# Kernel optimization log

Measured on AMD Instinct MI355X. Metric: run time of the kernel, lower is better.

The kernel has to match this reference:

```python
import jax, jax.numpy as jnp
import numpy as np

B, N, FD = 2, 50000, 13
E = 250000
M, H = 128, 128          # message_dim, hidden_dim
EDGE_IN = 2 * FD + 8     # 34
NODE_IN = FD + 2 * M     # 269


def _mlp(x, w1, b1, w2, b2):
    return jnp.tanh(x @ w1 + b1) @ w2 + b2


def setup_inputs() -> dict:
    root = jax.random.key(0)
    k = lambda i: jax.random.fold_in(root, i)

    def lin(i, din, dout):
        w = jax.random.normal(k(i), (din, dout), jnp.float32) * np.float32(1.0 / np.sqrt(din))
        b = jax.random.normal(k(i + 100), (dout,), jnp.float32) * np.float32(0.01)
        return w, b

    ew1, eb1 = lin(1, EDGE_IN, H); ew2, eb2 = lin(2, H, M)      # mlp_edge
    ww1, wb1 = lin(3, EDGE_IN, H); ww2, wb2 = lin(4, H, 1)      # mlp_weight
    xw1, xb1 = lin(5, EDGE_IN, H); xw2, xb2 = lin(6, H, M)      # mlp_edge_world
    yw1, yb1 = lin(7, EDGE_IN, H); yw2, yb2 = lin(8, H, 1)      # mlp_weight_world
    nw1, nb1 = lin(9, NODE_IN, H); nw2, nb2 = lin(10, H, FD)    # mlp_node

    z_h = jax.random.normal(k(20), (B, N, FD), jnp.float32)
    edge_hh = jax.random.randint(k(21), (B, 2, E), 0, N, jnp.int32)
    edge_world = jax.random.randint(k(22), (B, 2, E), 0, N, jnp.int32)
    return dict(z_h=z_h, edge_hh=edge_hh, edge_world=edge_world,
                ew1=ew1, eb1=eb1, ew2=ew2, eb2=eb2,
                ww1=ww1, wb1=wb1, ww2=ww2, wb2=wb2,
                xw1=xw1, xb1=xb1, xw2=xw2, xb2=xb2,
                yw1=yw1, yb1=yb1, yw2=yw2, yb2=yb2,
                nw1=nw1, nb1=nb1, nw2=nw2, nb2=nb2)


def _edge_features(z, s, t):
    # z: (N, FD); s, t: (E,)
    pos, vel = z[:, 0:3], z[:, 3:6]
    diff = pos[s] - pos[t]                               # (E, 3)
    dist = jnp.sum(diff * diff, axis=-1, keepdims=True)  # (E, 1) squared distance
    vxc = jnp.cross(vel[s], vel[t])                      # (E, 3)
    vxn = jnp.linalg.norm(vxc, axis=-1, keepdims=True)   # (E, 1)
    return jnp.concatenate([diff, dist, vxc, vxn], axis=-1)  # (E, 8)


def reference(z_h, edge_hh, edge_world,
              ew1, eb1, ew2, eb2, ww1, wb1, ww2, wb2,
              xw1, xb1, xw2, xb2, yw1, yb1, yw2, yb2,
              nw1, nb1, nw2, nb2):
    n_nodes = z_h.shape[1]

    def per_batch(z, e_hh, e_w):
        # normal edges
        s, t = e_hh[0], e_hh[1]
        inp = jnp.concatenate([z[s], z[t], _edge_features(z, s, t)], axis=-1)  # (E, 34)
        m = _mlp(inp, ew1, eb1, ew2, eb2)                                       # (E, M)
        w = jax.nn.sigmoid(_mlp(inp, ww1, wb1, ww2, wb2))                       # (E, 1)
        agg_h = jnp.zeros((n_nodes, M), z.dtype).at[t].add(w * m)
        # world edges
        sw, tw = e_w[0], e_w[1]
        inpw = jnp.concatenate([z[sw], z[tw], _edge_features(z, sw, tw)], axis=-1)
        mw = _mlp(inpw, xw1, xb1, xw2, xb2)
        ww_ = jax.nn.sigmoid(_mlp(inpw, yw1, yb1, yw2, yb2))
        agg_w = jnp.zeros((n_nodes, M), z.dtype).at[tw].add(ww_ * mw)
        return agg_h, agg_w

    m_agg_h, m_agg_w = jax.vmap(per_batch)(z_h, edge_hh, edge_world)  # (B, N, M) each
    input_node = jnp.concatenate([z_h, m_agg_h, m_agg_w], axis=-1)    # (B, N, 269)
    delta_z_h = _mlp(input_node, nw1, nb1, nw2, nb2)                  # (B, N, 13)
    return delta_z_h
```

## Files before the change

kernel.cpp:

```cpp
#include <hip/hip_runtime.h>
#include <hip/hip_bf16.h>

#define B_   2
#define N_   50000
#define FD_  13
#define E_   250000
#define M_   128
#define H_   128

typedef __attribute__((ext_vector_type(8))) short  short8;
typedef __attribute__((ext_vector_type(8))) __bf16 bf16x8;
typedef __attribute__((ext_vector_type(4))) float  f32x4;
typedef __attribute__((ext_vector_type(4))) unsigned int uint4v;
typedef __attribute__((ext_vector_type(8))) unsigned short ushort8;

#define AGG_BYTES  (4ull * N_ * 128 * 4)
#define HIST_BYTES (4ull * N_ * 4)
#define SORT_BYTES (4ull * E_ * 4)
#define OFF_EW1 0u
#define OFF_WW1 8192u
#define OFF_EW2 16384u
#define OFF_XW1 32768u
#define OFF_YW1 40960u
#define OFF_XW2 49152u
#define OFF_NW1 65536u
#define OFF_NW2 102400u

__device__ __forceinline__ float bf2f(unsigned short u) {
    unsigned int v = ((unsigned int)u) << 16;
    return __builtin_bit_cast(float, v);
}
__device__ __forceinline__ unsigned short f2bf(float f) {
    __bf16 h = (__bf16)f;
    return __builtin_bit_cast(unsigned short, h);
}
__device__ __forceinline__ float tanh_fast(float x) {
    float e = __builtin_amdgcn_exp2f(x * 2.8853900817779268f);
    float r = __builtin_amdgcn_rcpf(e + 1.0f);
    return __builtin_fmaf(-2.0f, r, 1.0f);
}
__device__ __forceinline__ float sigmoid_fast(float x) {
    float e = __builtin_amdgcn_exp2f(x * -1.4426950408889634f);
    return __builtin_amdgcn_rcpf(1.0f + e);
}
__device__ __forceinline__ f32x4 mfma16(short8 a, short8 b, f32x4 c) {
    return __builtin_amdgcn_mfma_f32_16x16x32_bf16(
        __builtin_bit_cast(bf16x8, a), __builtin_bit_cast(bf16x8, b), c, 0, 0, 0);
}

__global__ void prep_kernel(const float* __restrict__ ew1, const float* __restrict__ ww1,
                            const float* __restrict__ ew2, const float* __restrict__ xw1,
                            const float* __restrict__ yw1, const float* __restrict__ xw2,
                            const float* __restrict__ nw1, const float* __restrict__ nw2,
                            unsigned short* __restrict__ fb, uint4v* __restrict__ hist4) {
    int m = blockIdx.y, f = blockIdx.x, l = threadIdx.x;
    {
        unsigned int flat = ((unsigned int)m * gridDim.x + (unsigned int)f) * 64u + (unsigned int)l;
        const uint4v zv = {0u, 0u, 0u, 0u};
        for (unsigned int i = flat; i < 50000u; i += gridDim.x * gridDim.y * 64u)
            hist4[i] = zv;
    }
    const float* src; int K, Nn, KS; unsigned int off;
    switch (m) {
        case 0: src = ew1; K = 34;  Nn = 128; KS = 2; off = OFF_EW1; break;
        case 1: src = ww1; K = 34;  Nn = 128; KS = 2; off = OFF_WW1; break;
        case 2: src = ew2; K = 128; Nn = 128; KS = 4; off = OFF_EW2; break;
        case 3: src = xw1; K = 34;  Nn = 128; KS = 2; off = OFF_XW1; break;
        case 4: src = yw1; K = 34;  Nn = 128; KS = 2; off = OFF_YW1; break;
        case 5: src = xw2; K = 128; Nn = 128; KS = 4; off = OFF_XW2; break;
        case 6: src = nw1; K = 269; Nn = 128; KS = 9; off = OFF_NW1; break;
        default: src = nw2; K = 128; Nn = 13; KS = 4; off = OFF_NW2; break;
    }
    int NT = (Nn + 15) / 16;
    if (f >= KS * NT) return;
    int ks = f / NT, nt = f % NT;
    int n = nt * 16 + (l & 15);
    unsigned short* dst = fb + off + ((unsigned int)f * 64u + (unsigned int)l) * 8u;
    #pragma unroll
    for (int j = 0; j < 8; j++) {
        int k = ks * 32 + ((l >> 4) * 8) + j;
        int kk = k; bool valid = (k < K) && (n < Nn);
        if (m == 6) {
            if (k < 256)      kk = k + 13;
            else if (k < 269) kk = k - 256;
            else              valid = false;
            valid = valid && (n < Nn);
        }
        dst[j] = valid ? f2bf(src[kk * Nn + n]) : (unsigned short)0;
    }
}

__global__ void hist_kernel(const int* __restrict__ ehh, const int* __restrict__ eww,
                            int* __restrict__ hist) {
    int p = blockIdx.y, idx = blockIdx.x * 256 + threadIdx.x;
    if (idx >= E_) return;
    const int* eg = ((p >> 1) ? eww : ehh) + (size_t)(p & 1) * 2 * E_;
    atomicAdd(&hist[p * N_ + eg[E_ + idx]], 1);
}

__global__ void scan_kernel(int* __restrict__ hist) {
    __shared__ int part[1024];
    const int p = blockIdx.x, tid = threadIdx.x;
    int* h = hist + p * N_;
    const int lo = tid * 52;
    int cnt = N_ - lo; if (cnt < 0) cnt = 0; if (cnt > 52) cnt = 52;
    int v[52];
    int sum = 0;
    if (cnt == 52) {
        const int4* src = (const int4*)(h + lo);
        #pragma unroll
        for (int i = 0; i < 13; i++) {
            int4 t = src[i];
            v[4*i] = t.x; v[4*i+1] = t.y; v[4*i+2] = t.z; v[4*i+3] = t.w;
        }
        #pragma unroll
        for (int i = 0; i < 52; i++) sum += v[i];
    } else {
        for (int i = 0; i < cnt; i++) sum += h[lo + i];
    }
    part[tid] = sum;
    __syncthreads();
    for (int off = 1; off < 1024; off <<= 1) {
        int t = (tid >= off) ? part[tid - off] : 0;
        __syncthreads();
        part[tid] += t;
        __syncthreads();
    }
    int excl = (tid == 0) ? 0 : part[tid - 1];
    if (cnt == 52) {
        int4* dst = (int4*)(h + lo);
        #pragma unroll
        for (int i = 0; i < 13; i++) {
            int4 o;
            o.x = excl; excl += v[4*i];
            o.y = excl; excl += v[4*i+1];
            o.z = excl; excl += v[4*i+2];
            o.w = excl; excl += v[4*i+3];
            dst[i] = o;
        }
    } else {
        for (int i = 0; i < cnt; i++) { int t = h[lo + i]; h[lo + i] = excl; excl += t; }
    }
}

__global__ void scatter_kernel(const int* __restrict__ ehh, const int* __restrict__ eww,
                               int* __restrict__ hist, unsigned int* __restrict__ sorted,
                               uint4v* __restrict__ agg4) {
    int p = blockIdx.y, idx = blockIdx.x * 256 + threadIdx.x;
    {
        unsigned int flat = ((unsigned int)p * gridDim.x + (unsigned int)blockIdx.x) * 256u
                          + (unsigned int)threadIdx.x;
        const unsigned int nthr = gridDim.x * gridDim.y * 256u;
        const uint4v zv = {0u, 0u, 0u, 0u};
        for (unsigned int i = flat; i < 6400000u; i += nthr) agg4[i] = zv;
    }
    if (idx >= E_) return;
    const int* eg = ((p >> 1) ? eww : ehh) + (size_t)(p & 1) * 2 * E_;
    int s = eg[idx];
    int t = eg[E_ + idx];
    int pos = atomicAdd(&hist[p * N_ + t], 1);
    sorted[(size_t)p * E_ + pos] = (unsigned int)s | ((unsigned int)t << 16);
}

__launch_bounds__(256, 3)
__global__ void edge_kernel_agg(const float* __restrict__ z,
                                const unsigned int* __restrict__ sorted,
                                const unsigned short* __restrict__ fb,
                                float* __restrict__ agg,
                                const float* __restrict__ eb1, const float* __restrict__ wb1,
                                const float* __restrict__ ww2, const float* __restrict__ wb2,
                                const float* __restrict__ eb2,
                                const float* __restrict__ xb1, const float* __restrict__ yb1,
                                const float* __restrict__ yw2, const float* __restrict__ yb2,
                                const float* __restrict__ xb2) {
    __shared__ alignas(16) unsigned short Abuf[128][48];
    __shared__ alignas(16) unsigned short Hbuf[128][136];
    __shared__ float w_acc[128];
    __shared__ int   tgt_s[128];

    const int tid  = threadIdx.x;
    const int lane = tid & 63, wv = tid >> 6, quad = lane >> 4, c = lane & 15;
    const int pass = blockIdx.y, b = pass & 1, set = pass >> 1;
    const int ebase = blockIdx.x * 128;

    const float* zb = z + (size_t)b * N_ * FD_;
    float* aggp = agg + (size_t)pass * N_ * 128;

    const short8* Fm1 = (const short8*)(fb + (set ? OFF_XW1 : OFF_EW1));
    const short8* Fw1 = (const short8*)(fb + (set ? OFF_YW1 : OFF_WW1));
    const short8* Fm2 = (const short8*)(fb + (set ? OFF_XW2 : OFF_EW2));
    const float* B1m = set ? xb1 : eb1;
    const float* B1w = set ? yb1 : wb1;
    const float* B2m = set ? xb2 : eb2;
    const float* Wv2 = set ? yw2 : ww2;
    const float wbias = (set ? yb2 : wb2)[0];

    const int nt0 = wv * 2;
    short8 bm[2][2], bw[2][2], b2f[2][4];
    float bias1m[2], bias1w[2], bias2m[2], w2v[2];
    #pragma unroll
    for (int i = 0; i < 2; i++) {
        int nt = nt0 + i, n = nt * 16 + c;
        #pragma unroll
        for (int ks = 0; ks < 2; ks++) { bm[i][ks] = Fm1[(ks * 8 + nt) * 64 + lane];
                                         bw[i][ks] = Fw1[(ks * 8 + nt) * 64 + lane]; }
        #pragma unroll
        for (int ks = 0; ks < 4; ks++) { b2f[i][ks] = Fm2[(ks * 8 + nt) * 64 + lane]; }
        bias1m[i] = B1m[n]; bias1w[i] = B1w[n];
        bias2m[i] = B2m[n]; w2v[i] = Wv2[n];
    }

    if (tid < 128) {
        const int e = tid;
        const int prt = e >> 4, pqd = (e >> 2) & 3, prr = e & 3;
        const int wpos = pqd * 32 + prt * 4 + prr;
        int sp = ebase + wpos;
        const bool valid = (sp < E_);
        if (!valid) sp = E_ - 1;
        unsigned int st = sorted[(size_t)pass * E_ + sp];
        int s = (int)(st & 0xffffu), t = (int)(st >> 16);
        tgt_s[e] = valid ? t : -1;
        w_acc[e] = 0.0f;
        const float* zs = zb + (size_t)s * 13;
        const float* zt = zb + (size_t)t * 13;
        float fs[13], ft[13];
        __builtin_memcpy(fs, zs, 13 * sizeof(float));
        __builtin_memcpy(ft, zt, 13 * sizeof(float));
        float d0 = fs[0] - ft[0], d1 = fs[1] - ft[1], d2 = fs[2] - ft[2];
        float dist = d0 * d0 + d1 * d1 + d2 * d2;
        float c0 = fs[4] * ft[5] - fs[5] * ft[4];
        float c1 = fs[5] * ft[3] - fs[3] * ft[5];
        float c2 = fs[3] * ft[4] - fs[4] * ft[3];
        float vxn = sqrtf(c0 * c0 + c1 * c1 + c2 * c2);
        unsigned short row[40];
        #pragma unroll
        for (int j = 0; j < 13; j++) { row[j] = f2bf(fs[j]); row[13 + j] = f2bf(ft[j]); }
        row[26] = f2bf(d0); row[27] = f2bf(d1); row[28] = f2bf(d2); row[29] = f2bf(dist);
        row[30] = f2bf(c0); row[31] = f2bf(c1); row[32] = f2bf(c2); row[33] = f2bf(vxn);
        #pragma unroll
        for (int j = 34; j < 40; j++) row[j] = 0;
        #pragma unroll
        for (int v = 0; v < 5; v++) {
            short8 sv;
            #pragma unroll
            for (int j = 0; j < 8; j++) sv[j] = (short)row[v * 8 + j];
            *((short8*)&Abuf[e][v * 8]) = sv;
        }
    }
    __syncthreads();

    #pragma unroll 4
    for (int rt = 0; rt < 8; rt++) {
        const unsigned short* ar = &Abuf[rt * 16 + c][0];
        short8 a0 = *((const short8*)(ar + quad * 8));
        short8 a1 = {};
        if (quad == 0) a1 = *((const short8*)(ar + 32));
        float wpart[4] = {0.f, 0.f, 0.f, 0.f};
        #pragma unroll
        for (int i = 0; i < 2; i++) {
            f32x4 accm = {bias1m[i], bias1m[i], bias1m[i], bias1m[i]};
            f32x4 accw = {bias1w[i], bias1w[i], bias1w[i], bias1w[i]};
            accm = mfma16(a0, bm[i][0], accm);
            accm = mfma16(a1, bm[i][1], accm);
            accw = mfma16(a0, bw[i][0], accw);
            accw = mfma16(a1, bw[i][1], accw);
            int n = (nt0 + i) * 16 + c;
            #pragma unroll
            for (int r = 0; r < 4; r++) {
                Hbuf[rt * 16 + quad * 4 + r][n] = f2bf(tanh_fast(accm[r]));
                wpart[r] += tanh_fast(accw[r]) * w2v[i];
            }
        }
        #pragma unroll
        for (int r = 0; r < 4; r++) {
            float v = wpart[r];
            v += __shfl_xor(v, 1); v += __shfl_xor(v, 2);
            v += __shfl_xor(v, 4); v += __shfl_xor(v, 8);
            if (c == r) atomicAdd(&w_acc[rt * 16 + quad * 4 + r], v);
        }
    }
    __syncthreads();
    if (tid < 128) w_acc[tid] = sigmoid_fast(w_acc[tid] + wbias);
    __syncthreads();

    {
        const int n0 = nt0 * 16 + c;
        const int n1 = n0 + 16;
        int   tp = -1;
        float va0 = 0.f, va1 = 0.f;
        bool  from_start = true;
        #pragma unroll 2
        for (int rt = 0; rt < 8; rt++) {
            const unsigned short* hr = &Hbuf[rt * 16 + c][0];
            short8 h0 = *((const short8*)(hr + quad * 8));
            short8 h1 = *((const short8*)(hr + 32 + quad * 8));
            short8 h2 = *((const short8*)(hr + 64 + quad * 8));
            short8 h3 = *((const short8*)(hr + 96 + quad * 8));
            f32x4 accA = {bias2m[0], bias2m[0], bias2m[0], bias2m[0]};
            f32x4 accB = {bias2m[1], bias2m[1], bias2m[1], bias2m[1]};
            accA = mfma16(h0, b2f[0][0], accA);
            accA = mfma16(h1, b2f[0][1], accA);
            accA = mfma16(h2, b2f[0][2], accA);
            accA = mfma16(h3, b2f[0][3], accA);
            accB = mfma16(h0, b2f[1][0], accB);
            accB = mfma16(h1, b2f[1][1], accB);
            accB = mfma16(h2, b2f[1][2], accB);
            accB = mfma16(h3, b2f[1][3], accB);
            const int elq = rt * 16 + quad * 4;
            #pragma unroll
            for (int r = 0; r < 4; r++) {
                const int row = elq + r;
                const int tg = tgt_s[row];
                const float g = w_acc[row];
                const float v0 = accA[r] * g;
                const float v1 = accB[r] * g;
                if (tg == tp) {
                    va0 += v0; va1 += v1;
                } else {
                    if (tp >= 0) {
                        float* dst = aggp + (size_t)tp * 128;
                        if (from_start) { atomicAdd(dst + n0, va0); atomicAdd(dst + n1, va1); }
                        else            { dst[n0] = va0; dst[n1] = va1; }
                    }
                    tp = tg; va0 = v0; va1 = v1;
                    from_start = (rt == 0 && r == 0);
                }
            }
        }
        if (tp >= 0) {
            float* dst = aggp + (size_t)tp * 128;
            atomicAdd(dst + n0, va0);
            atomicAdd(dst + n1, va1);
        }
    }
}

#define NODE_BLOCKS 1024
__launch_bounds__(256, 4)
__global__ void node_fused(const float* __restrict__ z,
                           const float* __restrict__ agg,
                           const unsigned short* __restrict__ fb,
                           const float* __restrict__ nb1,
                           const float* __restrict__ nb2,
                           float* __restrict__ out) {
    __shared__ alignas(16) unsigned short Abuf[2][16][296];
    __shared__ alignas(16) unsigned short Hbuf[16][136];

    const int tid  = threadIdx.x;
    const int lane = tid & 63, wv = tid >> 6, quad = lane >> 4, c = lane & 15;
    const int nl = tid >> 4, part = tid & 15;
    constexpr int NT_TILES = (B_ * N_) / 16;

    for (int j = tid; j < 2 * 16 * 19; j += 256) {
        int bufi = j / (16 * 19), jj = j % (16 * 19);
        Abuf[bufi][jj / 19][269 + jj % 19] = 0;
    }

    const short8* F1 = (const short8*)(fb + OFF_NW1);
    const short8* F2 = (const short8*)(fb + OFF_NW2);
    const int nt0 = wv * 2;
    const float b1a = nb1[nt0 * 16 + c];
    const float b1b = nb1[(nt0 + 1) * 16 + c];
    const float bias2 = (c < 13) ? nb2[c] : 0.0f;

    f32x4 pa0, pa1, pb0, pb1;
    float pz = 0.0f;

    int t = blockIdx.x;

    {
        const int g = t * 16 + nl;
        const int b = (g >= N_) ? 1 : 0;
        const int tt = g - b * N_;
        const float* ap0 = agg + ((size_t)b * N_ + tt) * 128 + part * 8;
        const float* ap1 = agg + ((size_t)(2 + b) * N_ + tt) * 128 + part * 8;
        pa0 = *(const f32x4*)(ap0); pa1 = *(const f32x4*)(ap0 + 4);
        pb0 = *(const f32x4*)(ap1); pb1 = *(const f32x4*)(ap1 + 4);
        if (tid < 208) pz = z[(size_t)(t * 16 + tid / 13) * 13 + (tid % 13)];
    }

    int buf = 0;
    for (; t < NT_TILES; t += NODE_BLOCKS) {
        const int g0 = t * 16;
        {
            ushort8 u;
            #pragma unroll
            for (int k = 0; k < 4; k++) { u[k] = f2bf(pa0[k]); u[4 + k] = f2bf(pa1[k]); }
            *((ushort8*)&Abuf[buf][nl][part * 8]) = u;
            #pragma unroll
            for (int k = 0; k < 4; k++) { u[k] = f2bf(pb0[k]); u[4 + k] = f2bf(pb1[k]); }
            *((ushort8*)&Abuf[buf][nl][128 + part * 8]) = u;
            if (tid < 208) Abuf[buf][tid / 13][256 + tid % 13] = f2bf(pz);
        }
        const int tn = t + NODE_BLOCKS;
        if (tn < NT_TILES) {
            const int g = tn * 16 + nl;
            const int b = (g >= N_) ? 1 : 0;
            const int tt = g - b * N_;
            const float* ap0 = agg + ((size_t)b * N_ + tt) * 128 + part * 8;
            const float* ap1 = agg + ((size_t)(2 + b) * N_ + tt) * 128 + part * 8;
            pa0 = *(const f32x4*)(ap0); pa1 = *(const f32x4*)(ap0 + 4);
            pb0 = *(const f32x4*)(ap1); pb1 = *(const f32x4*)(ap1 + 4);
            if (tid < 208) pz = z[(size_t)(tn * 16 + tid / 13) * 13 + (tid % 13)];
        }
        __syncthreads();

        {
            f32x4 acc0 = {b1a, b1a, b1a, b1a};
            f32x4 acc1 = {b1b, b1b, b1b, b1b};
            #pragma unroll
            for (int ks = 0; ks < 9; ks++) {
                short8 a = *((const short8*)(&Abuf[buf][c][0] + ks * 32 + quad * 8));
                acc0 = mfma16(a, F1[(ks * 8 + nt0) * 64 + lane], acc0);
                acc1 = mfma16(a, F1[(ks * 8 + nt0 + 1) * 64 + lane], acc1);
            }
            #pragma unroll
            for (int r = 0; r < 4; r++) {
                Hbuf[quad * 4 + r][nt0 * 16 + c]       = f2bf(tanh_fast(acc0[r]));
                Hbuf[quad * 4 + r][(nt0 + 1) * 16 + c] = f2bf(tanh_fast(acc1[r]));
            }
        }
        __syncthreads();

        if (wv == 0) {
            f32x4 acc = {bias2, bias2, bias2, bias2};
            #pragma unroll
            for (int ks = 0; ks < 4; ks++) {
                short8 h = *((const short8*)(&Hbuf[c][0] + ks * 32 + quad * 8));
                acc = mfma16(h, F2[ks * 64 + lane], acc);
            }
            #pragma unroll
            for (int r = 0; r < 4; r++) {
                int g = g0 + quad * 4 + r;
                if (c < 13) out[(size_t)g * 13 + c] = acc[r];
            }
        }
        buf ^= 1;
    }
}

extern "C" void kernel_launch(void* const* d_in, const int* in_sizes, int n_in,
                              void* d_out, int out_size, void* d_ws, size_t ws_size,
                              hipStream_t stream) {
    const float* z   = (const float*)d_in[0];
    const int* ehh   = (const int*)d_in[1];
    const int* eww   = (const int*)d_in[2];
    const float* ew1 = (const float*)d_in[3];
    const float* eb1 = (const float*)d_in[4];
    const float* ew2 = (const float*)d_in[5];
    const float* eb2 = (const float*)d_in[6];
    const float* ww1 = (const float*)d_in[7];
    const float* wb1 = (const float*)d_in[8];
    const float* ww2 = (const float*)d_in[9];
    const float* wb2 = (const float*)d_in[10];
    const float* xw1 = (const float*)d_in[11];
    const float* xb1 = (const float*)d_in[12];
    const float* xw2 = (const float*)d_in[13];
    const float* xb2 = (const float*)d_in[14];
    const float* yw1 = (const float*)d_in[15];
    const float* yb1 = (const float*)d_in[16];
    const float* yw2 = (const float*)d_in[17];
    const float* yb2 = (const float*)d_in[18];
    const float* nw1 = (const float*)d_in[19];
    const float* nb1 = (const float*)d_in[20];
    const float* nw2 = (const float*)d_in[21];
    const float* nb2 = (const float*)d_in[22];

    float* agg  = (float*)d_ws;
    int* hist   = (int*)((char*)d_ws + AGG_BYTES);
    unsigned int* sorted = (unsigned int*)((char*)d_ws + AGG_BYTES + HIST_BYTES);
    unsigned short* frag = (unsigned short*)((char*)d_ws + AGG_BYTES + HIST_BYTES + SORT_BYTES);

    prep_kernel<<<dim3(72, 8), 64, 0, stream>>>(ew1, ww1, ew2, xw1, yw1, xw2, nw1, nw2,
                                                frag, (uint4v*)hist);
    hist_kernel<<<dim3((E_ + 255) / 256, 4), 256, 0, stream>>>(ehh, eww, hist);
    scan_kernel<<<4, 1024, 0, stream>>>(hist);
    scatter_kernel<<<dim3((E_ + 255) / 256, 4), 256, 0, stream>>>(ehh, eww, hist, sorted,
                                                                  (uint4v*)agg);
    edge_kernel_agg<<<dim3((E_ + 127) / 128, 4), 256, 0, stream>>>(
        z, sorted, frag, agg,
        eb1, wb1, ww2, wb2, eb2,
        xb1, yb1, yw2, yb2, xb2);
    node_fused<<<NODE_BLOCKS, 256, 0, stream>>>(
        z, agg, frag, nb1, nb2, (float*)d_out);
}
```

Baseline: 396.0 us.

## Split edge gate MLP into separate kernel writing per-edge gates

Moves the sigmoid-gated weight MLP out of the fused edge kernel into a new gate_kernel that writes one gate value per sorted edge to a workspace buffer. The main edge kernel then reads that gate instead of computing it, which cuts its register and instruction load and may raise occupancy. In exchange the edge gather and feature build run twice, there is one extra launch, and the gates take an extra round trip through global memory.

```diff
diff --git a/kernel.cpp b/kernel.cpp
--- a/kernel.cpp
+++ b/kernel.cpp
@@ -17,6 +17,7 @@
 #define AGG_BYTES  (4ull * N_ * 128 * 4)
 #define HIST_BYTES (4ull * N_ * 4)
 #define SORT_BYTES (4ull * E_ * 4)
+#define GATE_BYTES (4ull * E_ * 4)
 #define OFF_EW1 0u
 #define OFF_WW1 8192u
 #define OFF_EW2 16384u
@@ -162,21 +163,17 @@
     sorted[(size_t)p * E_ + pos] = (unsigned int)s | ((unsigned int)t << 16);
 }
 
-__launch_bounds__(256, 3)
-__global__ void edge_kernel_agg(const float* __restrict__ z,
-                                const unsigned int* __restrict__ sorted,
-                                const unsigned short* __restrict__ fb,
-                                float* __restrict__ agg,
-                                const float* __restrict__ eb1, const float* __restrict__ wb1,
-                                const float* __restrict__ ww2, const float* __restrict__ wb2,
-                                const float* __restrict__ eb2,
-                                const float* __restrict__ xb1, const float* __restrict__ yb1,
-                                const float* __restrict__ yw2, const float* __restrict__ yb2,
-                                const float* __restrict__ xb2) {
+__launch_bounds__(256, 6)
+__global__ void gate_kernel(const float* __restrict__ z,
+                            const unsigned int* __restrict__ sorted,
+                            const unsigned short* __restrict__ fb,
+                            float* __restrict__ gate_g,
+                            const float* __restrict__ wb1, const float* __restrict__ ww2,
+                            const float* __restrict__ wb2,
+                            const float* __restrict__ yb1, const float* __restrict__ yw2,
+                            const float* __restrict__ yb2) {
     __shared__ alignas(16) unsigned short Abuf[128][48];
-    __shared__ alignas(16) unsigned short Hbuf[128][136];
     __shared__ float w_acc[128];
-    __shared__ int   tgt_s[128];
 
     const int tid  = threadIdx.x;
     const int lane = tid & 63, wv = tid >> 6, quad = lane >> 4, c = lane & 15;
@@ -184,30 +181,20 @@
     const int ebase = blockIdx.x * 128;
 
     const float* zb = z + (size_t)b * N_ * FD_;
-    float* aggp = agg + (size_t)pass * N_ * 128;
-
-    const short8* Fm1 = (const short8*)(fb + (set ? OFF_XW1 : OFF_EW1));
     const short8* Fw1 = (const short8*)(fb + (set ? OFF_YW1 : OFF_WW1));
-    const short8* Fm2 = (const short8*)(fb + (set ? OFF_XW2 : OFF_EW2));
-    const float* B1m = set ? xb1 : eb1;
     const float* B1w = set ? yb1 : wb1;
-    const float* B2m = set ? xb2 : eb2;
     const float* Wv2 = set ? yw2 : ww2;
     const float wbias = (set ? yb2 : wb2)[0];
 
     const int nt0 = wv * 2;
-    short8 bm[2][2], bw[2][2], b2f[2][4];
-    float bias1m[2], bias1w[2], bias2m[2], w2v[2];
+    short8 bw[2][2];
+    float bias1w[2], w2v[2];
     #pragma unroll
     for (int i = 0; i < 2; i++) {
         int nt = nt0 + i, n = nt * 16 + c;
         #pragma unroll
-        for (int ks = 0; ks < 2; ks++) { bm[i][ks] = Fm1[(ks * 8 + nt) * 64 + lane];
-                                         bw[i][ks] = Fw1[(ks * 8 + nt) * 64 + lane]; }
-        #pragma unroll
-        for (int ks = 0; ks < 4; ks++) { b2f[i][ks] = Fm2[(ks * 8 + nt) * 64 + lane]; }
-        bias1m[i] = B1m[n]; bias1w[i] = B1w[n];
-        bias2m[i] = B2m[n]; w2v[i] = Wv2[n];
+        for (int ks = 0; ks < 2; ks++) bw[i][ks] = Fw1[(ks * 8 + nt) * 64 + lane];
+        bias1w[i] = B1w[n]; w2v[i] = Wv2[n];
     }
 
     if (tid < 128) {
@@ -215,11 +202,9 @@
         const int prt = e >> 4, pqd = (e >> 2) & 3, prr = e & 3;
         const int wpos = pqd * 32 + prt * 4 + prr;
         int sp = ebase + wpos;
-        const bool valid = (sp < E_);
-        if (!valid) sp = E_ - 1;
+        if (sp >= E_) sp = E_ - 1;
         unsigned int st = sorted[(size_t)pass * E_ + sp];
         int s = (int)(st & 0xffffu), t = (int)(st >> 16);
-        tgt_s[e] = valid ? t : -1;
         w_acc[e] = 0.0f;
         const float* zs = zb + (size_t)s * 13;
         const float* zt = zb + (size_t)t * 13;
@@ -249,38 +234,134 @@
     }
     __syncthreads();
 
+    #pragma unroll 1
+    for (int rt = 0; rt < 8; rt++) {
+        const unsigned short* ar = &Abuf[rt * 16 + c][0];
+        short8 a0 = *((const short8*)(ar + quad * 8));
+        short8 a1 = {};
+        if (quad == 0) a1 = *((const short8*)(ar + 32));
+        float wpart[4] = {0.f, 0.f, 0.f, 0.f};
+        #pragma unroll
+        for (int i = 0; i < 2; i++) {
+            f32x4 accw = {bias1w[i], bias1w[i], bias1w[i], bias1w[i]};
+            accw = mfma16(a0, bw[i][0], accw);
+            accw = mfma16(a1, bw[i][1], accw);
+            #pragma unroll
+            for (int r = 0; r < 4; r++) wpart[r] += tanh_fast(accw[r]) * w2v[i];
+        }
+        #pragma unroll
+        for (int r = 0; r < 4; r++) {
+            float v = wpart[r];
+            v += __shfl_xor(v, 1); v += __shfl_xor(v, 2);
+            v += __shfl_xor(v, 4); v += __shfl_xor(v, 8);
+            if (c == r) atomicAdd(&w_acc[rt * 16 + quad * 4 + r], v);
+        }
+    }
+    __syncthreads();
+
+    if (tid < 128) {
+        const int prt = tid >> 4, pqd = (tid >> 2) & 3, prr = tid & 3;
+        const int wpos = pqd * 32 + prt * 4 + prr;
+        const int sp = ebase + wpos;
+        if (sp < E_) gate_g[(size_t)pass * E_ + sp] = sigmoid_fast(w_acc[tid] + wbias);
+    }
+}
+
+__launch_bounds__(256, 3)
+__global__ void edge_kernel_agg(const float* __restrict__ z,
+                                const unsigned int* __restrict__ sorted,
+                                const unsigned short* __restrict__ fb,
+                                const float* __restrict__ gate_g,
+                                float* __restrict__ agg,
+                                const float* __restrict__ eb1, const float* __restrict__ eb2,
+                                const float* __restrict__ xb1, const float* __restrict__ xb2) {
+    __shared__ alignas(16) unsigned short Abuf[128][48];
+    __shared__ alignas(16) unsigned short Hbuf[128][136];
+    __shared__ float w_acc[128];
+    __shared__ int   tgt_s[128];
+
+    const int tid  = threadIdx.x;
+    const int lane = tid & 63, wv = tid >> 6, quad = lane >> 4, c = lane & 15;
+    const int pass = blockIdx.y, b = pass & 1, set = pass >> 1;
+    const int ebase = blockIdx.x * 128;
+
+    const float* zb = z + (size_t)b * N_ * FD_;
+    float* aggp = agg + (size_t)pass * N_ * 128;
+
+    const short8* Fm1 = (const short8*)(fb + (set ? OFF_XW1 : OFF_EW1));
+    const short8* Fm2 = (const short8*)(fb + (set ? OFF_XW2 : OFF_EW2));
+    const float* B1m = set ? xb1 : eb1;
+    const float* B2m = set ? xb2 : eb2;
+
+    const int nt0 = wv * 2;
+    short8 bm[2][2], b2f[2][4];
+    float bias1m[2], bias2m[2];
+    #pragma unroll
+    for (int i = 0; i < 2; i++) {
+        int nt = nt0 + i, n = nt * 16 + c;
+        #pragma unroll
+        for (int ks = 0; ks < 2; ks++) bm[i][ks] = Fm1[(ks * 8 + nt) * 64 + lane];
+        #pragma unroll
+        for (int ks = 0; ks < 4; ks++) b2f[i][ks] = Fm2[(ks * 8 + nt) * 64 + lane];
+        bias1m[i] = B1m[n]; bias2m[i] = B2m[n];
+    }
+
+    if (tid < 128) {
+        const int e = tid;
+        const int prt = e >> 4, pqd = (e >> 2) & 3, prr = e & 3;
+        const int wpos = pqd * 32 + prt * 4 + prr;
+        int sp = ebase + wpos;
+        const bool valid = (sp < E_);
+        if (!valid) sp = E_ - 1;
+        unsigned int st = sorted[(size_t)pass * E_ + sp];
+        int s = (int)(st & 0xffffu), t = (int)(st >> 16);
+        tgt_s[e] = valid ? t : -1;
+        w_acc[e] = gate_g[(size_t)pass * E_ + sp];
+        const float* zs = zb + (size_t)s * 13;
+        const float* zt = zb + (size_t)t * 13;
+        float fs[13], ft[13];
+        __builtin_memcpy(fs, zs, 13 * sizeof(float));
+        __builtin_memcpy(ft, zt, 13 * sizeof(float));
+        float d0 = fs[0] - ft[0], d1 = fs[1] - ft[1], d2 = fs[2] - ft[2];
+        float dist = d0 * d0 + d1 * d1 + d2 * d2;
+        float c0 = fs[4] * ft[5] - fs[5] * ft[4];
+        float c1 = fs[5] * ft[3] - fs[3] * ft[5];
+        float c2 = fs[3] * ft[4] - fs[4] * ft[3];
+        float vxn = sqrtf(c0 * c0 + c1 * c1 + c2 * c2);
+        unsigned short row[40];
+        #pragma unroll
+        for (int j = 0; j < 13; j++) { row[j] = f2bf(fs[j]); row[13 + j] = f2bf(ft[j]); }
+        row[26] = f2bf(d0); row[27] = f2bf(d1); row[28] = f2bf(d2); row[29] = f2bf(dist);
+        row[30] = f2bf(c0); row[31] = f2bf(c1); row[32] = f2bf(c2); row[33] = f2bf(vxn);
+        #pragma unroll
+        for (int j = 34; j < 40; j++) row[j] = 0;
+        #pragma unroll
+        for (int v = 0; v < 5; v++) {
+            short8 sv;
+            #pragma unroll
+            for (int j = 0; j < 8; j++) sv[j] = (short)row[v * 8 + j];
+            *((short8*)&Abuf[e][v * 8]) = sv;
+        }
+    }
+    __syncthreads();
+
     #pragma unroll 4
     for (int rt = 0; rt < 8; rt++) {
         const unsigned short* ar = &Abuf[rt * 16 + c][0];
         short8 a0 = *((const short8*)(ar + quad * 8));
         short8 a1 = {};
         if (quad == 0) a1 = *((const short8*)(ar + 32));
-        float wpart[4] = {0.f, 0.f, 0.f, 0.f};
         #pragma unroll
         for (int i = 0; i < 2; i++) {
             f32x4 accm = {bias1m[i], bias1m[i], bias1m[i], bias1m[i]};
-            f32x4 accw = {bias1w[i], bias1w[i], bias1w[i], bias1w[i]};
             accm = mfma16(a0, bm[i][0], accm);
             accm = mfma16(a1, bm[i][1], accm);
-            accw = mfma16(a0, bw[i][0], accw);
-            accw = mfma16(a1, bw[i][1], accw);
             int n = (nt0 + i) * 16 + c;
             #pragma unroll
-            for (int r = 0; r < 4; r++) {
+            for (int r = 0; r < 4; r++)
                 Hbuf[rt * 16 + quad * 4 + r][n] = f2bf(tanh_fast(accm[r]));
-                wpart[r] += tanh_fast(accw[r]) * w2v[i];
-            }
-        }
-        #pragma unroll
-        for (int r = 0; r < 4; r++) {
-            float v = wpart[r];
-            v += __shfl_xor(v, 1); v += __shfl_xor(v, 2);
-            v += __shfl_xor(v, 4); v += __shfl_xor(v, 8);
-            if (c == r) atomicAdd(&w_acc[rt * 16 + quad * 4 + r], v);
-        }
-    }
-    __syncthreads();
-    if (tid < 128) w_acc[tid] = sigmoid_fast(w_acc[tid] + wbias);
+        }
+    }
     __syncthreads();
 
     {
@@ -469,7 +550,9 @@
     float* agg  = (float*)d_ws;
     int* hist   = (int*)((char*)d_ws + AGG_BYTES);
     unsigned int* sorted = (unsigned int*)((char*)d_ws + AGG_BYTES + HIST_BYTES);
-    unsigned short* frag = (unsigned short*)((char*)d_ws + AGG_BYTES + HIST_BYTES + SORT_BYTES);
+    float* gate = (float*)((char*)d_ws + AGG_BYTES + HIST_BYTES + SORT_BYTES);
+    unsigned short* frag = (unsigned short*)((char*)d_ws + AGG_BYTES + HIST_BYTES
+                                             + SORT_BYTES + GATE_BYTES);
 
     prep_kernel<<<dim3(72, 8), 64, 0, stream>>>(ew1, ww1, ew2, xw1, yw1, xw2, nw1, nw2,
                                                 frag, (uint4v*)hist);
@@ -477,10 +560,10 @@
     scan_kernel<<<4, 1024, 0, stream>>>(hist);
     scatter_kernel<<<dim3((E_ + 255) / 256, 4), 256, 0, stream>>>(ehh, eww, hist, sorted,
                                                                   (uint4v*)agg);
+    gate_kernel<<<dim3((E_ + 127) / 128, 4), 256, 0, stream>>>(
+        z, sorted, frag, gate, wb1, ww2, wb2, yb1, yw2, yb2);
     edge_kernel_agg<<<dim3((E_ + 127) / 128, 4), 256, 0, stream>>>(
-        z, sorted, frag, agg,
-        eb1, wb1, ww2, wb2, eb2,
-        xb1, yb1, yw2, yb2, xb2);
+        z, sorted, frag, gate, agg, eb1, eb2, xb1, xb2);
     node_fused<<<NODE_BLOCKS, 256, 0, stream>>>(
         z, agg, frag, nb1, nb2, (float*)d_out);
 }
```

Result: no change. 401.5 us (+1.4%).
